# Optimization experiments

Hardware: AMD Instinct MI355X
Metric: run time of the kernel (lower is better)

## Reference

```python
import jax, jax.numpy as jnp
import numpy as np

N_NODES = 100000
N_EDGES = 1250000
IN_CH = 64
HID_CH = 64
OUT_CH = 64
N_GRAPHS = 128


def gcn_conv(x, W, b, src, dst, num_nodes):
    """PyG GCNConv: out = D^{-1/2} (A + I) D^{-1/2} X W + b.

    src/dst already include self-loops. Messages flow src -> dst,
    aggregated (scatter-add) at dst.
    """
    xw = x @ W  # [N, out]
    deg = jax.ops.segment_sum(jnp.ones_like(dst, dtype=x.dtype), dst,
                              num_segments=num_nodes)  # [N], >=1 from self-loops
    dinv = jax.lax.rsqrt(deg)
    norm = dinv[src] * dinv[dst]  # [E+N]
    msgs = xw[src] * norm[:, None]  # gather + scale
    out = jax.ops.segment_sum(msgs, dst, num_segments=num_nodes)  # scatter-add
    return out + b


def setup_inputs() -> dict:
    key = jax.random.key(0)
    ks = jax.random.split(key, 10)
    x = jax.random.normal(ks[0], (N_NODES, IN_CH), dtype=jnp.float32)
    edge_index = jax.random.randint(ks[1], (2, N_EDGES), 0, N_NODES, dtype=jnp.int64)
    batch = jnp.sort(jax.random.randint(ks[2], (N_NODES,), 0, N_GRAPHS, dtype=jnp.int64))
    # Glorot-ish init for weights, zeros for biases (PyG/torch defaults)
    def glorot(k, fan_in, fan_out):
        s = np.sqrt(6.0 / (fan_in + fan_out)).astype(np.float32)
        return jax.random.uniform(k, (fan_in, fan_out), dtype=jnp.float32,
                                  minval=-s, maxval=s)
    W1 = glorot(ks[3], IN_CH, HID_CH)
    b1 = jnp.zeros((HID_CH,), dtype=jnp.float32)
    W2 = glorot(ks[4], HID_CH, OUT_CH)
    b2 = jnp.zeros((OUT_CH,), dtype=jnp.float32)
    Wfc = glorot(ks[5], OUT_CH, OUT_CH)
    bfc = jnp.zeros((OUT_CH,), dtype=jnp.float32)
    return {"x": x, "edge_index": edge_index, "batch": batch,
            "W1": W1, "b1": b1, "W2": W2, "b2": b2, "Wfc": Wfc, "bfc": bfc}


def reference(x, edge_index, batch, W1, b1, W2, b2, Wfc, bfc):
    num_nodes = x.shape[0]
    # add self-loops once; reused by both conv layers
    loop = jnp.arange(num_nodes, dtype=edge_index.dtype)
    src = jnp.concatenate([edge_index[0], loop])
    dst = jnp.concatenate([edge_index[1], loop])

    h = jax.nn.relu(gcn_conv(x, W1, b1, src, dst, num_nodes))
    h = jax.nn.relu(gcn_conv(h, W2, b2, src, dst, num_nodes))

    # global_mean_pool over batch segment ids
    sums = jax.ops.segment_sum(h, batch, num_segments=N_GRAPHS)  # [B, out]
    counts = jax.ops.segment_sum(jnp.ones((num_nodes,), dtype=h.dtype), batch,
                                 num_segments=N_GRAPHS)
    pooled = sums / jnp.maximum(counts, 1.0)[:, None]

    return jax.nn.relu(pooled @ Wfc + bfc)
```

## Files before the change

### kernel.cpp

```cpp
#include <hip/hip_runtime.h>
#include <hip/hip_fp16.h>
#include <type_traits>

#define NCH 64
#define MAXB 512
#define CHUNK 4096
#define POOL_BLOCKS 2048

typedef _Float16 half8 __attribute__((ext_vector_type(8)));
typedef float floatx4 __attribute__((ext_vector_type(4)));

__global__ __launch_bounds__(256) void bucket_hist(const int* __restrict__ dst, int E,
                                                   int NB, int* __restrict__ bhist) {
    __shared__ int lh[MAXB];
    int t = threadIdx.x;
    for (int i = t; i < NB; i += 256) lh[i] = 0;
    __syncthreads();
    int base = blockIdx.x * CHUNK;
    int end = min(base + CHUNK, E);
    for (int i = base + t; i < end; i += 256)
        atomicAdd(&lh[dst[i] >> 8], 1);
    __syncthreads();
    for (int i = t; i < NB; i += 256) {
        int v = lh[i];
        if (v) atomicAdd(&bhist[i], v);
    }
}

__global__ __launch_bounds__(MAXB) void bucket_scan(const int* __restrict__ bhist, int NB,
                                                    int* __restrict__ bbase,
                                                    int* __restrict__ bcursor) {
    __shared__ int s[MAXB];
    int t = threadIdx.x;
    int v = (t < NB) ? bhist[t] : 0;
    s[t] = v;
    __syncthreads();
    for (int o = 1; o < MAXB; o <<= 1) {
        int x = (t >= o) ? s[t - o] : 0;
        __syncthreads();
        s[t] += x;
        __syncthreads();
    }
    int excl = s[t] - v;
    if (t < NB) { bbase[t] = excl; bcursor[t] = excl; }
    if (t == NB - 1) bbase[NB] = s[t];
}

__global__ __launch_bounds__(256) void bucket_scatter(const int* __restrict__ src,
                                                      const int* __restrict__ dst, int E,
                                                      int NB, int* __restrict__ bcursor,
                                                      int* __restrict__ tmp) {
    __shared__ int lh[MAXB];
    __shared__ int lbase[MAXB];
    int t = threadIdx.x;
    for (int i = t; i < NB; i += 256) lh[i] = 0;
    __syncthreads();
    int base = blockIdx.x * CHUNK;
    int end = min(base + CHUNK, E);
    for (int i = base + t; i < end; i += 256)
        atomicAdd(&lh[dst[i] >> 8], 1);
    __syncthreads();
    for (int i = t; i < NB; i += 256) {
        int v = lh[i];
        lbase[i] = v ? atomicAdd(&bcursor[i], v) : 0;
        lh[i] = 0;
    }
    __syncthreads();
    for (int i = base + t; i < end; i += 256) {
        int s_ = src[i], d_ = dst[i];
        int b = d_ >> 8;
        int p = lbase[b] + atomicAdd(&lh[b], 1);
        tmp[p] = (s_ << 8) | (d_ & 255);
    }
}

__global__ __launch_bounds__(256) void bucket_finalize(const int* __restrict__ tmp,
                                                       const int* __restrict__ bbase,
                                                       int n, int E, int NB,
                                                       int* __restrict__ offsets,
                                                       float* __restrict__ dinv,
                                                       int* __restrict__ srcs) {
    int b = blockIdx.x;
    int t = threadIdx.x;
    __shared__ int ldeg[256];
    __shared__ int lsc[256];
    __shared__ int lcur[256];
    ldeg[t] = 0;
    __syncthreads();
    int s0 = bbase[b], e0 = bbase[b + 1];
    for (int e = s0 + t; e < e0; e += 256)
        atomicAdd(&ldeg[tmp[e] & 255], 1);
    __syncthreads();
    int v = ldeg[t];
    lsc[t] = v;
    __syncthreads();
    for (int o = 1; o < 256; o <<= 1) {
        int x = (t >= o) ? lsc[t - o] : 0;
        __syncthreads();
        lsc[t] += x;
        __syncthreads();
    }
    int excl = lsc[t] - v;
    lcur[t] = excl;
    int node = (b << 8) + t;
    if (node < n) {
        offsets[node] = s0 + excl;
        dinv[node] = rsqrtf((float)v + 1.0f);
    }
    if (b == NB - 1 && t == 0) offsets[n] = E;
    __syncthreads();
    for (int e = s0 + t; e < e0; e += 256) {
        int r = tmp[e];
        int p = s0 + atomicAdd(&lcur[r & 255], 1);
        srcs[p] = (int)(((unsigned)r) >> 8) << 7;
    }
}

__global__ __launch_bounds__(256) void convert_wt(const float* __restrict__ W1,
                                                  const float* __restrict__ W2,
                                                  _Float16* __restrict__ wt1,
                                                  _Float16* __restrict__ wt2) {
    int idx = blockIdx.x * 256 + threadIdx.x;
    int j = idx & 4095;
    int k = j >> 6, c = j & 63;
    if (idx < 4096) wt1[c * NCH + k] = (_Float16)W1[j];
    else            wt2[c * NCH + k] = (_Float16)W2[j];
}

template <typename T>
__global__ __launch_bounds__(256) void gemm64_mfma(const T* __restrict__ X,
                                                   const _Float16* __restrict__ wt,
                                                   const float* __restrict__ dscale,
                                                   __half* __restrict__ Y, int n) {
    int tid = threadIdx.x;
    int lane = tid & 63, wv = tid >> 6;
    int row0 = blockIdx.x * 64 + wv * 16;
    if (row0 >= n) return;

    int lrow = lane & 15;
    int kgrp = (lane >> 4) * 8;

    half8 bf[4][2];
#pragma unroll
    for (int ct = 0; ct < 4; ++ct) {
#pragma unroll
        for (int ks = 0; ks < 2; ++ks) {
            bf[ct][ks] = *(const half8*)(wt + (ct * 16 + lrow) * NCH + ks * 32 + kgrp);
        }
    }

    int arow = row0 + lrow;
    half8 af[2];
    if constexpr (std::is_same_v<T, float>) {
        if (arow < n) {
#pragma unroll
            for (int ks = 0; ks < 2; ++ks) {
                const float4* xr = (const float4*)(X + (arow << 6) + ks * 32 + kgrp);
                float4 u0 = xr[0], u1 = xr[1];
                half8 a;
                a[0] = (_Float16)u0.x; a[1] = (_Float16)u0.y;
                a[2] = (_Float16)u0.z; a[3] = (_Float16)u0.w;
                a[4] = (_Float16)u1.x; a[5] = (_Float16)u1.y;
                a[6] = (_Float16)u1.z; a[7] = (_Float16)u1.w;
                af[ks] = a;
            }
        } else {
            af[0] = half8{}; af[1] = half8{};
        }
    } else {
        if (arow < n) {
#pragma unroll
            for (int ks = 0; ks < 2; ++ks)
                af[ks] = *(const half8*)((const _Float16*)X + (arow << 6) + ks * 32 + kgrp);
        } else {
            af[0] = half8{}; af[1] = half8{};
        }
    }

    floatx4 acc[4] = {floatx4{0,0,0,0}, floatx4{0,0,0,0}, floatx4{0,0,0,0}, floatx4{0,0,0,0}};
#pragma unroll
    for (int ks = 0; ks < 2; ++ks) {
#pragma unroll
        for (int ct = 0; ct < 4; ++ct) {
            acc[ct] = __builtin_amdgcn_mfma_f32_16x16x32_f16(af[ks], bf[ct][ks], acc[ct], 0, 0, 0);
        }
    }

    int rbase = row0 + (lane >> 4) * 4;
    float ds[4];
#pragma unroll
    for (int i = 0; i < 4; ++i) ds[i] = (rbase + i < n) ? dscale[rbase + i] : 0.f;
#pragma unroll
    for (int i = 0; i < 4; ++i) {
        int row = rbase + i;
        if (row < n) {
#pragma unroll
            for (int ct = 0; ct < 4; ++ct) {
                Y[(row << 6) + ct * 16 + lrow] = __float2half(acc[ct][i] * ds[i]);
            }
        }
    }
}

__global__ __launch_bounds__(256) void gather_fused(const __half* __restrict__ XWs,
                                                    const int* __restrict__ srcs,
                                                    const int* __restrict__ offsets,
                                                    const float* __restrict__ dinv,
                                                    const float* __restrict__ b,
                                                    __half* __restrict__ H, int n) {
    int wid  = (blockIdx.x * 256 + threadIdx.x) >> 6;
    int lane = threadIdx.x & 63;
    if (wid >= n) return;
    const char* tab = (const char*)(XWs + lane);
    int start = offsets[wid], end = offsets[wid + 1];
    float acc0 = __half2float(*(const __half*)(tab + (wid << 7)));
    float acc1 = 0.f, acc2 = 0.f, acc3 = 0.f;
    int e = start;
    for (; e + 8 <= end; e += 8) {
        int o0 = srcs[e],     o1 = srcs[e + 1], o2 = srcs[e + 2], o3 = srcs[e + 3];
        int o4 = srcs[e + 4], o5 = srcs[e + 5], o6 = srcs[e + 6], o7 = srcs[e + 7];
        acc0 += __half2float(*(const __half*)(tab + o0));
        acc1 += __half2float(*(const __half*)(tab + o1));
        acc2 += __half2float(*(const __half*)(tab + o2));
        acc3 += __half2float(*(const __half*)(tab + o3));
        acc0 += __half2float(*(const __half*)(tab + o4));
        acc1 += __half2float(*(const __half*)(tab + o5));
        acc2 += __half2float(*(const __half*)(tab + o6));
        acc3 += __half2float(*(const __half*)(tab + o7));
    }
    for (; e + 2 <= end; e += 2) {
        int o0 = srcs[e], o1 = srcs[e + 1];
        acc0 += __half2float(*(const __half*)(tab + o0));
        acc1 += __half2float(*(const __half*)(tab + o1));
    }
    if (e < end) {
        int o0 = srcs[e];
        acc2 += __half2float(*(const __half*)(tab + o0));
    }
    float v = (acc0 + acc1) + (acc2 + acc3);
    v = v * dinv[wid] + b[lane];
    H[(wid << 6) + lane] = __float2half(v > 0.0f ? v : 0.0f);
}

__global__ __launch_bounds__(256) void pool_partial(const __half* __restrict__ H,
                                                    const int* __restrict__ batch, int n,
                                                    float* __restrict__ pooled) {
    int gwave = blockIdx.x * 4 + (threadIdx.x >> 6);
    int lane  = threadIdx.x & 63;
    int nwaves = POOL_BLOCKS * 4;
    int per = (n + nwaves - 1) / nwaves;
    int start = gwave * per;
    int end = min(start + per, n);
    if (start >= end) return;
    int cur = batch[start];
    float acc = 0.f;
    for (int i = start; i < end; ++i) {
        int g = batch[i];
        if (g != cur) {
            atomicAdd(&pooled[(cur << 6) + lane], acc);
            acc = 0.f;
            cur = g;
        }
        acc += __half2float(H[(i << 6) + lane]);
    }
    atomicAdd(&pooled[(cur << 6) + lane], acc);
}

__global__ __launch_bounds__(64) void fc_out(const float* __restrict__ pooled,
                                             const int* __restrict__ batch, int n,
                                             const float* __restrict__ Wfc,
                                             const float* __restrict__ bfc,
                                             float* __restrict__ out) {
    int g = blockIdx.x;
    int c = threadIdx.x;
    int lo = 0, hi = n;
    while (lo < hi) { int m = (lo + hi) >> 1; if (batch[m] < g) lo = m + 1; else hi = m; }
    int start = lo;
    hi = n;
    while (lo < hi) { int m = (lo + hi) >> 1; if (batch[m] < g + 1) lo = m + 1; else hi = m; }
    int count = lo - start;

    __shared__ float ps[64];
    float inv = 1.0f / (float)(count > 1 ? count : 1);
    ps[c] = pooled[(g << 6) + c] * inv;
    __syncthreads();
    float acc = bfc[c];
#pragma unroll
    for (int k = 0; k < 64; ++k) acc += ps[k] * Wfc[k * NCH + c];
    out[(g << 6) + c] = acc > 0.0f ? acc : 0.0f;
}

static inline size_t align256(size_t x) { return (x + 255) & ~(size_t)255; }

extern "C" void kernel_launch(void* const* d_in, const int* in_sizes, int n_in,
                              void* d_out, int out_size, void* d_ws, size_t ws_size,
                              hipStream_t stream) {
    const float* x     = (const float*)d_in[0];
    const int*   ei    = (const int*)d_in[1];
    const int*   batch = (const int*)d_in[2];
    const float* W1    = (const float*)d_in[3];
    const float* b1    = (const float*)d_in[4];
    const float* W2    = (const float*)d_in[5];
    const float* b2    = (const float*)d_in[6];
    const float* Wfc   = (const float*)d_in[7];
    const float* bfc   = (const float*)d_in[8];
    float* out = (float*)d_out;

    int E = in_sizes[1] / 2;
    int n = in_sizes[0] / NCH;
    int ngraphs = out_size / NCH;
    const int* src = ei;
    const int* dst = ei + E;
    int NB = (n + 255) >> 8;

    char* p = (char*)d_ws;
    int*      bhist   = (int*)p;      p += align256((size_t)(MAXB + 1) * 4);
    int*      bbase   = (int*)p;      p += align256((size_t)(MAXB + 1) * 4);
    int*      bcursor = (int*)p;      p += align256((size_t)MAXB * 4);
    int*      offsets = (int*)p;      p += align256((size_t)(n + 1) * 4);
    float*    dinv    = (float*)p;    p += align256((size_t)n * 4);
    float*    pooled  = (float*)p;    p += align256((size_t)ngraphs * NCH * 4);
    _Float16* wt1     = (_Float16*)p; p += align256((size_t)NCH * NCH * 2);
    _Float16* wt2     = (_Float16*)p; p += align256((size_t)NCH * NCH * 2);
    int*      tmp     = (int*)p;      p += align256((size_t)E * 4);
    int*      srcs    = (int*)p;      p += align256((size_t)E * 4);
    __half*   xwh     = (__half*)p;   p += align256((size_t)n * NCH * 2);
    __half*   h       = (__half*)p;

    int eblocks = (E + CHUNK - 1) / CHUNK;

    hipMemsetAsync(bhist, 0, (size_t)NB * sizeof(int), stream);
    hipMemsetAsync(pooled, 0, (size_t)ngraphs * NCH * sizeof(float), stream);
    convert_wt<<<32, 256, 0, stream>>>(W1, W2, wt1, wt2);
    bucket_hist<<<eblocks, 256, 0, stream>>>(dst, E, NB, bhist);
    bucket_scan<<<1, MAXB, 0, stream>>>(bhist, NB, bbase, bcursor);
    bucket_scatter<<<eblocks, 256, 0, stream>>>(src, dst, E, NB, bcursor, tmp);
    bucket_finalize<<<NB, 256, 0, stream>>>(tmp, bbase, n, E, NB, offsets, dinv, srcs);

    int gemm_blocks = (n + 63) / 64;

    gemm64_mfma<float><<<gemm_blocks, 256, 0, stream>>>(x, wt1, dinv, xwh, n);
    gather_fused<<<(n * NCH + 255) / 256, 256, 0, stream>>>(xwh, srcs, offsets, dinv, b1, h, n);

    gemm64_mfma<__half><<<gemm_blocks, 256, 0, stream>>>(h, wt2, dinv, xwh, n);
    gather_fused<<<(n * NCH + 255) / 256, 256, 0, stream>>>(xwh, srcs, offsets, dinv, b2, h, n);

    pool_partial<<<POOL_BLOCKS, 256, 0, stream>>>(h, batch, n, pooled);
    fc_out<<<ngraphs, 64, 0, stream>>>(pooled, batch, n, Wfc, bfc, out);
}
```

Measured before the change: 278.0 us.

## Pad CSR neighbor lists to multiples of 16 and unroll gather by 16

Each node's adjacency list is padded to a multiple of 16 entries, with pad entries pointing at a zero row appended after the XW table. Offsets are packed as base and iteration count in one int. This lets the gather loop run fixed 16-wide unrolled iterations with no remainder handling, exposing more independent loads. It also merges the weight conversion and the two memsets into one prep kernel, dropping two launches. The cost is extra padded edges, about 6 on average for degree around 13, which adds memory traffic. The zero-row reads mostly hit cache.

```diff
diff --git a/kernel.cpp b/kernel.cpp
--- a/kernel.cpp
+++ b/kernel.cpp
@@ -6,9 +6,31 @@
 #define MAXB 512
 #define CHUNK 4096
 #define POOL_BLOCKS 2048
+#define PADMAX 3840
 
 typedef _Float16 half8 __attribute__((ext_vector_type(8)));
 typedef float floatx4 __attribute__((ext_vector_type(4)));
+
+__global__ __launch_bounds__(256) void prep(const float* __restrict__ W1,
+                                            const float* __restrict__ W2,
+                                            _Float16* __restrict__ wt1,
+                                            _Float16* __restrict__ wt2,
+                                            int* __restrict__ bhist, int NB,
+                                            float* __restrict__ pooled, int npool,
+                                            __half* __restrict__ xwhz) {
+    int i = blockIdx.x * 256 + threadIdx.x;
+    if (i < 4096) {
+        int k = i >> 6, c = i & 63;
+        wt1[c * NCH + k] = (_Float16)W1[i];
+    } else if (i < 8192) {
+        int j = i - 4096;
+        int k = j >> 6, c = j & 63;
+        wt2[c * NCH + k] = (_Float16)W2[j];
+    }
+    if (i <= NB) bhist[i] = 0;
+    if (i < npool) pooled[i] = 0.f;
+    if (i < 64) xwhz[i] = __float2half(0.f);
+}
 
 __global__ __launch_bounds__(256) void bucket_hist(const int* __restrict__ dst, int E,
                                                    int NB, int* __restrict__ bhist) {
@@ -76,7 +98,7 @@
 
 __global__ __launch_bounds__(256) void bucket_finalize(const int* __restrict__ tmp,
                                                        const int* __restrict__ bbase,
-                                                       int n, int E, int NB,
+                                                       int n, int NB, int zoff,
                                                        int* __restrict__ offsets,
                                                        float* __restrict__ dinv,
                                                        int* __restrict__ srcs) {
@@ -91,8 +113,9 @@
     for (int e = s0 + t; e < e0; e += 256)
         atomicAdd(&ldeg[tmp[e] & 255], 1);
     __syncthreads();
-    int v = ldeg[t];
-    lsc[t] = v;
+    int d = ldeg[t];
+    int pd = (d + 15) & ~15;
+    lsc[t] = pd;
     __syncthreads();
     for (int o = 1; o < 256; o <<= 1) {
         int x = (t >= o) ? lsc[t - o] : 0;
@@ -100,31 +123,22 @@
         lsc[t] += x;
         __syncthreads();
     }
-    int excl = lsc[t] - v;
-    lcur[t] = excl;
+    int pexcl = lsc[t] - pd;
+    lcur[t] = pexcl;
+    int s0p = s0 + b * PADMAX;
     int node = (b << 8) + t;
     if (node < n) {
-        offsets[node] = s0 + excl;
-        dinv[node] = rsqrtf((float)v + 1.0f);
-    }
-    if (b == NB - 1 && t == 0) offsets[n] = E;
+        offsets[node] = ((s0p + pexcl) << 8) | (pd >> 4);
+        dinv[node] = rsqrtf((float)d + 1.0f);
+    }
     __syncthreads();
     for (int e = s0 + t; e < e0; e += 256) {
         int r = tmp[e];
-        int p = s0 + atomicAdd(&lcur[r & 255], 1);
-        srcs[p] = (int)(((unsigned)r) >> 8) << 7;
-    }
-}
-
-__global__ __launch_bounds__(256) void convert_wt(const float* __restrict__ W1,
-                                                  const float* __restrict__ W2,
-                                                  _Float16* __restrict__ wt1,
-                                                  _Float16* __restrict__ wt2) {
-    int idx = blockIdx.x * 256 + threadIdx.x;
-    int j = idx & 4095;
-    int k = j >> 6, c = j & 63;
-    if (idx < 4096) wt1[c * NCH + k] = (_Float16)W1[j];
-    else            wt2[c * NCH + k] = (_Float16)W2[j];
+        int p = s0p + atomicAdd(&lcur[r & 255], 1);
+        srcs[p] = ((int)(((unsigned)r) >> 8)) << 7;
+    }
+    __syncthreads();
+    for (int q = pexcl + d; q < pexcl + pd; ++q) srcs[s0p + q] = zoff;
 }
 
 template <typename T>
@@ -155,7 +169,7 @@
         if (arow < n) {
 #pragma unroll
             for (int ks = 0; ks < 2; ++ks) {
-                const float4* xr = (const float4*)(X + (arow << 6) + ks * 32 + kgrp);
+                const float4* xr = (const float4*)(X + ((size_t)arow << 6) + ks * 32 + kgrp);
                 float4 u0 = xr[0], u1 = xr[1];
                 half8 a;
                 a[0] = (_Float16)u0.x; a[1] = (_Float16)u0.y;
@@ -171,7 +185,7 @@
         if (arow < n) {
 #pragma unroll
             for (int ks = 0; ks < 2; ++ks)
-                af[ks] = *(const half8*)((const _Float16*)X + (arow << 6) + ks * 32 + kgrp);
+                af[ks] = *(const half8*)((const _Float16*)X + ((size_t)arow << 6) + ks * 32 + kgrp);
         } else {
             af[0] = half8{}; af[1] = half8{};
         }
@@ -196,7 +210,7 @@
         if (row < n) {
 #pragma unroll
             for (int ct = 0; ct < 4; ++ct) {
-                Y[(row << 6) + ct * 16 + lrow] = __float2half(acc[ct][i] * ds[i]);
+                Y[((size_t)row << 6) + ct * 16 + lrow] = __float2half(acc[ct][i] * ds[i]);
             }
         }
     }
@@ -212,34 +226,38 @@
     int lane = threadIdx.x & 63;
     if (wid >= n) return;
     const char* tab = (const char*)(XWs + lane);
-    int start = offsets[wid], end = offsets[wid + 1];
-    float acc0 = __half2float(*(const __half*)(tab + (wid << 7)));
-    float acc1 = 0.f, acc2 = 0.f, acc3 = 0.f;
-    int e = start;
-    for (; e + 8 <= end; e += 8) {
-        int o0 = srcs[e],     o1 = srcs[e + 1], o2 = srcs[e + 2], o3 = srcs[e + 3];
-        int o4 = srcs[e + 4], o5 = srcs[e + 5], o6 = srcs[e + 6], o7 = srcs[e + 7];
-        acc0 += __half2float(*(const __half*)(tab + o0));
-        acc1 += __half2float(*(const __half*)(tab + o1));
-        acc2 += __half2float(*(const __half*)(tab + o2));
-        acc3 += __half2float(*(const __half*)(tab + o3));
-        acc0 += __half2float(*(const __half*)(tab + o4));
-        acc1 += __half2float(*(const __half*)(tab + o5));
-        acc2 += __half2float(*(const __half*)(tab + o6));
-        acc3 += __half2float(*(const __half*)(tab + o7));
-    }
-    for (; e + 2 <= end; e += 2) {
-        int o0 = srcs[e], o1 = srcs[e + 1];
-        acc0 += __half2float(*(const __half*)(tab + o0));
-        acc1 += __half2float(*(const __half*)(tab + o1));
-    }
-    if (e < end) {
-        int o0 = srcs[e];
-        acc2 += __half2float(*(const __half*)(tab + o0));
-    }
-    float v = (acc0 + acc1) + (acc2 + acc3);
-    v = v * dinv[wid] + b[lane];
-    H[(wid << 6) + lane] = __float2half(v > 0.0f ? v : 0.0f);
+    int pk = offsets[wid];
+    int base = pk >> 8;
+    int nit = pk & 255;
+    float dv = dinv[wid];
+    float bias = b[lane];
+    float self = __half2float(*(const __half*)(tab + (wid << 7)));
+    float a0 = 0.f, a1 = 0.f, a2 = 0.f, a3 = 0.f;
+    for (int it = 0; it < nit; ++it) {
+        int e = base + (it << 4);
+        float t0  = __half2float(*(const __half*)(tab + srcs[e + 0]));
+        float t1  = __half2float(*(const __half*)(tab + srcs[e + 1]));
+        float t2  = __half2float(*(const __half*)(tab + srcs[e + 2]));
+        float t3  = __half2float(*(const __half*)(tab + srcs[e + 3]));
+        float t4  = __half2float(*(const __half*)(tab + srcs[e + 4]));
+        float t5  = __half2float(*(const __half*)(tab + srcs[e + 5]));
+        float t6  = __half2float(*(const __half*)(tab + srcs[e + 6]));
+        float t7  = __half2float(*(const __half*)(tab + srcs[e + 7]));
+        float t8  = __half2float(*(const __half*)(tab + srcs[e + 8]));
+        float t9  = __half2float(*(const __half*)(tab + srcs[e + 9]));
+        float t10 = __half2float(*(const __half*)(tab + srcs[e + 10]));
+        float t11 = __half2float(*(const __half*)(tab + srcs[e + 11]));
+        float t12 = __half2float(*(const __half*)(tab + srcs[e + 12]));
+        float t13 = __half2float(*(const __half*)(tab + srcs[e + 13]));
+        float t14 = __half2float(*(const __half*)(tab + srcs[e + 14]));
+        float t15 = __half2float(*(const __half*)(tab + srcs[e + 15]));
+        a0 += t0 + t4 + t8  + t12;
+        a1 += t1 + t5 + t9  + t13;
+        a2 += t2 + t6 + t10 + t14;
+        a3 += t3 + t7 + t11 + t15;
+    }
+    float v = (self + ((a0 + a1) + (a2 + a3))) * dv + bias;
+    H[((size_t)wid << 6) + lane] = __float2half(v > 0.0f ? v : 0.0f);
 }
 
 __global__ __launch_bounds__(256) void pool_partial(const __half* __restrict__ H,
@@ -261,7 +279,7 @@
             acc = 0.f;
             cur = g;
         }
-        acc += __half2float(H[(i << 6) + lane]);
+        acc += __half2float(H[((size_t)i << 6) + lane]);
     }
     atomicAdd(&pooled[(cur << 6) + lane], acc);
 }
@@ -312,6 +330,7 @@
     const int* src = ei;
     const int* dst = ei + E;
     int NB = (n + 255) >> 8;
+    int npool = ngraphs * NCH;
 
     char* p = (char*)d_ws;
     int*      bhist   = (int*)p;      p += align256((size_t)(MAXB + 1) * 4);
@@ -319,23 +338,22 @@
     int*      bcursor = (int*)p;      p += align256((size_t)MAXB * 4);
     int*      offsets = (int*)p;      p += align256((size_t)(n + 1) * 4);
     float*    dinv    = (float*)p;    p += align256((size_t)n * 4);
-    float*    pooled  = (float*)p;    p += align256((size_t)ngraphs * NCH * 4);
+    float*    pooled  = (float*)p;    p += align256((size_t)npool * 4);
     _Float16* wt1     = (_Float16*)p; p += align256((size_t)NCH * NCH * 2);
     _Float16* wt2     = (_Float16*)p; p += align256((size_t)NCH * NCH * 2);
     int*      tmp     = (int*)p;      p += align256((size_t)E * 4);
-    int*      srcs    = (int*)p;      p += align256((size_t)E * 4);
-    __half*   xwh     = (__half*)p;   p += align256((size_t)n * NCH * 2);
+    int*      srcs    = (int*)p;      p += align256((size_t)(E + (size_t)NB * PADMAX) * 4);
+    __half*   xwh     = (__half*)p;   p += align256(((size_t)n + 1) * NCH * 2);
     __half*   h       = (__half*)p;
 
     int eblocks = (E + CHUNK - 1) / CHUNK;
-
-    hipMemsetAsync(bhist, 0, (size_t)NB * sizeof(int), stream);
-    hipMemsetAsync(pooled, 0, (size_t)ngraphs * NCH * sizeof(float), stream);
-    convert_wt<<<32, 256, 0, stream>>>(W1, W2, wt1, wt2);
+    int zoff = n << 7;
+
+    prep<<<32, 256, 0, stream>>>(W1, W2, wt1, wt2, bhist, NB, pooled, npool, xwh + (size_t)n * NCH);
     bucket_hist<<<eblocks, 256, 0, stream>>>(dst, E, NB, bhist);
     bucket_scan<<<1, MAXB, 0, stream>>>(bhist, NB, bbase, bcursor);
     bucket_scatter<<<eblocks, 256, 0, stream>>>(src, dst, E, NB, bcursor, tmp);
-    bucket_finalize<<<NB, 256, 0, stream>>>(tmp, bbase, n, E, NB, offsets, dinv, srcs);
+    bucket_finalize<<<NB, 256, 0, stream>>>(tmp, bbase, n, NB, zoff, offsets, dinv, srcs);
 
     int gemm_blocks = (n + 63) / 64;
 
```

Result: faster. 243.4 us (-12.5%).
